# Performance work log

Measured on AMD Instinct MI355X. Metric: run time of the kernel, lower is better.

The kernel has to match this reference:

```python
import jax, jax.numpy as jnp
import numpy as np

NACT = 4  # len(activation_list): [linear, cos, sin, tan]


def setup_inputs() -> dict:
    key = jax.random.key(0)
    kx, kw = jax.random.split(key)
    size_in, size_out, batch = 256, 1024, 131072
    x = jax.random.normal(kx, (batch, size_in), dtype=jnp.float32)
    # kaiming_uniform_ with a=sqrt(5): bound = sqrt(6/((1+a^2)*fan_in)) = 1/sqrt(fan_in)
    bound = 1.0 / np.sqrt(size_in)
    weight = jax.random.uniform(kw, (size_out, size_in), dtype=jnp.float32,
                                minval=-bound, maxval=bound)
    return {"x": x, "weight": weight}


def reference(x, weight):
    # linear_combo = x @ W^T : [B, size_out]
    y = jnp.matmul(x, weight.T)
    B, O = y.shape
    # Column j gets activation_list[j % NACT]; reshape so last axis = j % NACT.
    y3 = y.reshape(B, O // NACT, NACT)
    out = jnp.stack(
        [y3[..., 0],            # linear
         jnp.cos(y3[..., 1]),   # cos
         jnp.sin(y3[..., 2]),   # sin
         jnp.tan(y3[..., 3])],  # tan
        axis=-1,
    )
    return out.reshape(B, O)
```

## Files before the change

### kernel.cpp

```cpp
#include <hip/hip_runtime.h>
#include <math.h>

#define BATCH 131072
#define KDIM  256
#define ODIM  1024

#define BM 128
#define BN 128
#define BK 32
#define PAD 4

__global__ __launch_bounds__(256) void gemm_act(
    const float* __restrict__ x,
    const float* __restrict__ w,
    float* __restrict__ out)
{
    __shared__ float As[BK][BM + PAD];
    __shared__ float Bs[BK][BN + PAD];

    const int tid  = threadIdx.x;
    const int col0 = blockIdx.x * BN;
    const int row0 = blockIdx.y * BM;
    const int ty   = (tid >> 4) << 2;
    const int tx   = (tid & 15) << 2;

    float acc[8][8] = {};

    for (int k0 = 0; k0 < KDIM; k0 += BK) {
        #pragma unroll
        for (int l = 0; l < 4; ++l) {
            const int f  = tid + l * 256;
            const int r  = f >> 3;
            const int k4 = (f & 7) << 2;
            float4 va = *(const float4*)(x + (size_t)(row0 + r) * KDIM + k0 + k4);
            float4 vb = *(const float4*)(w + (size_t)(col0 + r) * KDIM + k0 + k4);
            As[k4 + 0][r] = va.x; As[k4 + 1][r] = va.y;
            As[k4 + 2][r] = va.z; As[k4 + 3][r] = va.w;
            Bs[k4 + 0][r] = vb.x; Bs[k4 + 1][r] = vb.y;
            Bs[k4 + 2][r] = vb.z; Bs[k4 + 3][r] = vb.w;
        }
        __syncthreads();

        #pragma unroll 8
        for (int k = 0; k < BK; ++k) {
            float4 a0 = *(const float4*)&As[k][ty];
            float4 a1 = *(const float4*)&As[k][64 + ty];
            float4 b0 = *(const float4*)&Bs[k][tx];
            float4 b1 = *(const float4*)&Bs[k][64 + tx];
            const float ar[8] = {a0.x, a0.y, a0.z, a0.w, a1.x, a1.y, a1.z, a1.w};
            const float br[8] = {b0.x, b0.y, b0.z, b0.w, b1.x, b1.y, b1.z, b1.w};
            #pragma unroll
            for (int i = 0; i < 8; ++i)
                #pragma unroll
                for (int j = 0; j < 8; ++j)
                    acc[i][j] = fmaf(ar[i], br[j], acc[i][j]);
        }
        __syncthreads();
    }

    #pragma unroll
    for (int i = 0; i < 8; ++i) {
        const int row = row0 + (i < 4 ? ty + i : 64 + ty + (i - 4));
        #pragma unroll
        for (int jh = 0; jh < 2; ++jh) {
            const int colb = col0 + jh * 64 + tx;
            const float y0 = acc[i][jh * 4 + 0];
            const float y1 = acc[i][jh * 4 + 1];
            const float y2 = acc[i][jh * 4 + 2];
            const float y3 = acc[i][jh * 4 + 3];

            float4 o;
            o.x = y0;
            o.y = __cosf(y1);
            o.z = __sinf(y2);
            o.w = tanf(y3);

            const float m    = rintf(y3 * 0.31830988618379067f);
            const float r_   = fmaf(-m, 3.14159265358979323f, y3);
            const float dist = fabsf(fabsf(r_) - 1.57079632679489662f);
            if (dist < 1e-2f) {
                o.w = (float)tan((double)y3);
            }

            *(float4*)(out + (size_t)row * ODIM + colb) = o;
        }
    }
}

extern "C" void kernel_launch(void* const* d_in, const int* in_sizes, int n_in,
                              void* d_out, int out_size, void* d_ws, size_t ws_size,
                              hipStream_t stream)
{
    const float* x = (const float*)d_in[0];
    const float* w = (const float*)d_in[1];
    float* out = (float*)d_out;

    dim3 grid(ODIM / BN, BATCH / BM);
    gemm_act<<<grid, 256, 0, stream>>>(x, w, out);
}
```

Measured before the change: 1.262 ms.

## Prefetch next K-tile into registers and use nontemporal output stores

Global loads for the next K tile now go into registers while the current tile is being computed, which overlaps memory latency with FMA work. The sync barriers are restructured so there is one before the shared-memory writes and one after. The output stores become nontemporal so the large result does not pollute the cache. In exchange the prefetch buffers use 32 more registers per thread, which can lower occupancy.

Measured after the change: 1.318 ms. +4.5%, slower.

```diff
diff --git a/kernel.cpp b/kernel.cpp
--- a/kernel.cpp
+++ b/kernel.cpp
@@ -9,6 +9,9 @@
 #define BN 128
 #define BK 32
 #define PAD 4
+#define NT (KDIM / BK)
+
+typedef float vfloat4 __attribute__((ext_vector_type(4)));
 
 __global__ __launch_bounds__(256) void gemm_act(
     const float* __restrict__ x,
@@ -24,21 +27,42 @@
     const int ty   = (tid >> 4) << 2;
     const int tx   = (tid & 15) << 2;
 
+    const int r_ = tid >> 3;
+    const int k4 = (tid & 7) << 2;
+
+    const float* xp = x + (size_t)(row0 + r_) * KDIM + k4;
+    const float* wp = w + (size_t)(col0 + r_) * KDIM + k4;
+
+    float4 pa[4], pb[4];
+    #pragma unroll
+    for (int l = 0; l < 4; ++l) {
+        pa[l] = *(const float4*)(xp + (size_t)(l * 32) * KDIM);
+        pb[l] = *(const float4*)(wp + (size_t)(l * 32) * KDIM);
+    }
+
     float acc[8][8] = {};
 
-    for (int k0 = 0; k0 < KDIM; k0 += BK) {
+    for (int t = 0; t < NT; ++t) {
+        __syncthreads();
+
         #pragma unroll
         for (int l = 0; l < 4; ++l) {
-            const int f  = tid + l * 256;
-            const int r  = f >> 3;
-            const int k4 = (f & 7) << 2;
-            float4 va = *(const float4*)(x + (size_t)(row0 + r) * KDIM + k0 + k4);
-            float4 vb = *(const float4*)(w + (size_t)(col0 + r) * KDIM + k0 + k4);
-            As[k4 + 0][r] = va.x; As[k4 + 1][r] = va.y;
-            As[k4 + 2][r] = va.z; As[k4 + 3][r] = va.w;
-            Bs[k4 + 0][r] = vb.x; Bs[k4 + 1][r] = vb.y;
-            Bs[k4 + 2][r] = vb.z; Bs[k4 + 3][r] = vb.w;
+            const int r = r_ + l * 32;
+            As[k4 + 0][r] = pa[l].x; As[k4 + 1][r] = pa[l].y;
+            As[k4 + 2][r] = pa[l].z; As[k4 + 3][r] = pa[l].w;
+            Bs[k4 + 0][r] = pb[l].x; Bs[k4 + 1][r] = pb[l].y;
+            Bs[k4 + 2][r] = pb[l].z; Bs[k4 + 3][r] = pb[l].w;
         }
+
+        if (t + 1 < NT) {
+            const int k0n = (t + 1) * BK;
+            #pragma unroll
+            for (int l = 0; l < 4; ++l) {
+                pa[l] = *(const float4*)(xp + k0n + (size_t)(l * 32) * KDIM);
+                pb[l] = *(const float4*)(wp + k0n + (size_t)(l * 32) * KDIM);
+            }
+        }
+
         __syncthreads();
 
         #pragma unroll 8
@@ -55,7 +79,6 @@
                 for (int j = 0; j < 8; ++j)
                     acc[i][j] = fmaf(ar[i], br[j], acc[i][j]);
         }
-        __syncthreads();
     }
 
     #pragma unroll
@@ -69,20 +92,20 @@
             const float y2 = acc[i][jh * 4 + 2];
             const float y3 = acc[i][jh * 4 + 3];
 
-            float4 o;
+            vfloat4 o;
             o.x = y0;
             o.y = __cosf(y1);
             o.z = __sinf(y2);
             o.w = tanf(y3);
 
             const float m    = rintf(y3 * 0.31830988618379067f);
-            const float r_   = fmaf(-m, 3.14159265358979323f, y3);
-            const float dist = fabsf(fabsf(r_) - 1.57079632679489662f);
+            const float r2   = fmaf(-m, 3.14159265358979323f, y3);
+            const float dist = fabsf(fabsf(r2) - 1.57079632679489662f);
             if (dist < 1e-2f) {
                 o.w = (float)tan((double)y3);
             }
 
-            *(float4*)(out + (size_t)row * ODIM + colb) = o;
+            __builtin_nontemporal_store(o, (vfloat4*)(out + (size_t)row * ODIM + colb));
         }
     }
 }
```
